# Kernel optimization log

Hardware: AMD Instinct MI355X
Metric: run time of the kernel (lower is better)

Reference implementation:

```python
import jax, jax.numpy as jnp
import numpy as np


def setup_inputs() -> dict:
    key = jax.random.key(0)
    k1, k2, k3 = jax.random.split(key, 3)
    d_in, d_sae, N = 2048, 16384, 8192
    x = jax.random.normal(k1, (N, d_in), dtype=jnp.float32)
    W_enc = jax.random.normal(k2, (d_in, d_sae), dtype=jnp.float32) * (1.0 / np.sqrt(d_in))
    W_dec = jax.random.normal(k3, (d_sae, d_in), dtype=jnp.float32)
    # normalize decoder rows (SAE convention; check_decoder_norms expects unit rows)
    W_dec = W_dec / jnp.linalg.norm(W_dec, axis=1, keepdims=True)
    b_enc = jnp.zeros((d_sae,), dtype=jnp.float32)
    b_dec = jnp.zeros((d_in,), dtype=jnp.float32)
    return {"x": x, "W_enc": W_enc, "W_dec": W_dec, "b_enc": b_enc, "b_dec": b_dec, "k": 64}


def reference(x, W_enc, W_dec, b_enc, b_dec, k):
    # encode: dense matmul then top-k masking with ReLU on kept activations
    pre_acts = x @ W_enc + b_enc                      # [N, d_sae]
    top_acts, top_idx = jax.lax.top_k(pre_acts, k)    # [N, k] each
    N = pre_acts.shape[0]
    rows = jnp.arange(N)[:, None]                     # [N, 1]
    acts = jnp.zeros_like(pre_acts).at[rows, top_idx].set(jax.nn.relu(top_acts))
    # decode
    recon = acts @ W_dec + b_dec                      # [N, d_in]
    return recon
```

## Files before the change

kernel.cpp:

```cpp
#include <hip/hip_runtime.h>

#define M_ROWS 8192
#define K_DIM  2048
#define N_SAE  16384
#define TOPK   64
#define WEPS   0.027f

typedef __attribute__((ext_vector_type(8))) short bf16x8;
typedef __attribute__((ext_vector_type(4))) float f32x4;

__device__ __forceinline__ unsigned short f2bf(float f) {
  unsigned u = __float_as_uint(f);
  u += 0x7FFFu + ((u >> 16) & 1u);
  return (unsigned short)(u >> 16);
}

__device__ __forceinline__ float key2float(unsigned k) {
  unsigned short bits = (k & 0x8000u) ? (unsigned short)(k ^ 0x8000u)
                                      : (unsigned short)(~k);
  _Float16 h;
  __builtin_memcpy(&h, &bits, 2);
  return (float)h;
}

__device__ __forceinline__ void gload16(const void* g, void* l) {
  __builtin_amdgcn_global_load_lds(
      (const __attribute__((address_space(1))) unsigned int*)g,
      (__attribute__((address_space(3))) unsigned int*)l, 16, 0, 0);
}

__global__ __launch_bounds__(256) void k_convx(const float* __restrict__ x,
                                               unsigned short* __restrict__ xb) {
  const long i = ((long)blockIdx.x * 256 + threadIdx.x) * 4;
  float4 v = *(const float4*)(x + i);
  ushort4 o;
  o.x = f2bf(v.x); o.y = f2bf(v.y); o.z = f2bf(v.z); o.w = f2bf(v.w);
  *(ushort4*)(xb + i) = o;
}

__global__ __launch_bounds__(256) void k_transpose(const float* __restrict__ W,
                                                   float* __restrict__ Wt,
                                                   unsigned short* __restrict__ Wtb) {
  __shared__ float tile[32][33];
  const int nb = blockIdx.x * 32;
  const int kb = blockIdx.y * 32;
  const int tx = threadIdx.x & 31;
  const int ty = threadIdx.x >> 5;
#pragma unroll
  for (int i = 0; i < 32; i += 8)
    tile[ty + i][tx] = W[(long)(kb + ty + i) * N_SAE + nb + tx];
  __syncthreads();
#pragma unroll
  for (int i = 0; i < 32; i += 8) {
    float v = tile[tx][ty + i];
    long o = (long)(nb + ty + i) * K_DIM + kb + tx;
    Wt[o] = v;
    Wtb[o] = f2bf(v);
  }
}

__global__ __launch_bounds__(256) void k_gemm(const unsigned short* __restrict__ A,
                                              const unsigned short* __restrict__ B,
                                              const float* __restrict__ b_enc,
                                              _Float16* __restrict__ C) {
  __shared__ unsigned short As[128 * 32];
  __shared__ unsigned short Bs[128 * 32];
  const int t = threadIdx.x;
  const int lane = t & 63;
  const int wave = t >> 6;
  const int wm = wave >> 1, wn = wave & 1;
  const int bm = blockIdx.y * 128, bn = blockIdx.x * 128;
  f32x4 acc[4][4] = {};

  const int c0 = t, c1 = t + 256;
  const unsigned short* a0 = A + (long)(bm + (c0 >> 2)) * K_DIM + (c0 & 3) * 8;
  const unsigned short* a1 = A + (long)(bm + (c1 >> 2)) * K_DIM + (c1 & 3) * 8;
  const unsigned short* b0 = B + (long)(bn + (c0 >> 2)) * K_DIM + (c0 & 3) * 8;
  const unsigned short* b1 = B + (long)(bn + (c1 >> 2)) * K_DIM + (c1 & 3) * 8;
  unsigned short* la0 = As + c0 * 8;
  unsigned short* la1 = As + c1 * 8;
  unsigned short* lb0 = Bs + c0 * 8;
  unsigned short* lb1 = Bs + c1 * 8;

  const int kh = lane >> 4;
  const int ml = lane & 15;

  for (int k0 = 0; k0 < K_DIM; k0 += 32) {
    __syncthreads();
    gload16(a0 + k0, la0);
    gload16(a1 + k0, la1);
    gload16(b0 + k0, lb0);
    gload16(b1 + k0, lb1);
    __syncthreads();
    bf16x8 af[4], bfr[4];
#pragma unroll
    for (int i = 0; i < 4; i++)
      af[i] = *(const bf16x8*)(As + (wm * 64 + i * 16 + ml) * 32 + kh * 8);
#pragma unroll
    for (int j = 0; j < 4; j++)
      bfr[j] = *(const bf16x8*)(Bs + (wn * 64 + j * 16 + ml) * 32 + kh * 8);
#pragma unroll
    for (int i = 0; i < 4; i++)
#pragma unroll
      for (int j = 0; j < 4; j++)
        acc[i][j] = __builtin_amdgcn_mfma_f32_16x16x32_bf16(af[i], bfr[j], acc[i][j], 0, 0, 0);
  }
#pragma unroll
  for (int j = 0; j < 4; j++) {
    const int gn = bn + wn * 64 + j * 16 + ml;
    const float bias = b_enc[gn];
#pragma unroll
    for (int i = 0; i < 4; i++) {
      const int gm0 = bm + wm * 64 + i * 16 + kh * 4;
#pragma unroll
      for (int r = 0; r < 4; r++)
        C[(long)(gm0 + r) * N_SAE + gn] = (_Float16)(acc[i][j][r] + bias);
    }
  }
}

__global__ __launch_bounds__(256) void k_select(const unsigned short* __restrict__ pre,
                                                int* __restrict__ def_idx,
                                                int* __restrict__ amb_idx,
                                                int* __restrict__ counts) {
  __shared__ unsigned short keys[16384];
  __shared__ unsigned int hist[256];
  __shared__ unsigned int scan[256];
  __shared__ unsigned int sc[8];
  const long row = blockIdx.x;
  const int t = threadIdx.x;
  const uint4* src = (const uint4*)(pre + row * N_SAE);
  uint4* kdst = (uint4*)keys;
#pragma unroll
  for (int i = 0; i < 8; i++) {
    uint4 v = src[i * 256 + t];
    uint4 o;
    unsigned s;
    s = v.x & 0x80008000u; o.x = v.x ^ (0x80008000u | ((s >> 15) * 0x7FFFu));
    s = v.y & 0x80008000u; o.y = v.y ^ (0x80008000u | ((s >> 15) * 0x7FFFu));
    s = v.z & 0x80008000u; o.z = v.z ^ (0x80008000u | ((s >> 15) * 0x7FFFu));
    s = v.w & 0x80008000u; o.w = v.w ^ (0x80008000u | ((s >> 15) * 0x7FFFu));
    kdst[i * 256 + t] = o;
  }
  hist[t] = 0;
  if (t < 8) sc[t] = 0;
  __syncthreads();
  for (int i = 0; i < 64; i++) {
    unsigned k = keys[i * 256 + t];
    atomicAdd(&hist[k >> 8], 1u);
  }
  __syncthreads();
  scan[t] = hist[t];
  __syncthreads();
  for (int off = 1; off < 256; off <<= 1) {
    unsigned v = (t + off < 256) ? scan[t + off] : 0u;
    __syncthreads();
    scan[t] += v;
    __syncthreads();
  }
  if (scan[t] >= TOPK && (t == 255 || scan[t + 1] < TOPK)) {
    sc[0] = (unsigned)t;
    sc[1] = (t == 255) ? 0u : scan[t + 1];
  }
  __syncthreads();
  const unsigned bstar = sc[0];
  const unsigned H = sc[1];
  hist[t] = 0;
  __syncthreads();
  for (int i = 0; i < 64; i++) {
    unsigned k = keys[i * 256 + t];
    if ((k >> 8) == bstar) atomicAdd(&hist[k & 255u], 1u);
  }
  __syncthreads();
  scan[t] = hist[t];
  __syncthreads();
  for (int off = 1; off < 256; off <<= 1) {
    unsigned v = (t + off < 256) ? scan[t + off] : 0u;
    __syncthreads();
    scan[t] += v;
    __syncthreads();
  }
  if (H + scan[t] >= TOPK && (t == 255 || H + scan[t + 1] < TOPK)) sc[2] = (unsigned)t;
  __syncthreads();
  const unsigned T = (bstar << 8) | sc[2];
  const float tf = key2float(T);
  const float lo = tf - WEPS;
  const float hi = tf + WEPS;
  for (int i = 0; i < 64; i++) {
    unsigned k = keys[i * 256 + t];
    float vf = key2float(k);
    if (vf > hi) {
      unsigned p = atomicAdd(&sc[3], 1u);
      def_idx[row * 64 + p] = i * 256 + t;
    } else if (vf >= lo) {
      unsigned p = atomicAdd(&sc[4], 1u);
      if (p < 64) amb_idx[row * 64 + p] = i * 256 + t;
    }
  }
  __syncthreads();
  if (t == 0) {
    counts[row * 2]     = (int)sc[3];
    counts[row * 2 + 1] = (int)(sc[4] < 64u ? sc[4] : 64u);
  }
}

__global__ __launch_bounds__(256) void k_exact2(const float* __restrict__ x,
                                                const float* __restrict__ Wt,
                                                const float* __restrict__ b_enc,
                                                const _Float16* __restrict__ pre,
                                                const int* __restrict__ def_idx,
                                                const int* __restrict__ amb_idx,
                                                const int* __restrict__ counts,
                                                int* __restrict__ tidx,
                                                float* __restrict__ tact) {
  __shared__ float xs[2048];
  __shared__ double vals[64];
  __shared__ int idxs[64];
  const int row = blockIdx.x;
  const int t = threadIdx.x;
  {
    const float4* src = (const float4*)(x + (long)row * K_DIM);
    ((float4*)xs)[t] = src[t];
    ((float4*)xs)[t + 256] = src[t + 256];
  }
  const int ndef = counts[row * 2];
  const int namb = counts[row * 2 + 1];
  if (t < 64) {
    idxs[t] = (t < namb) ? amb_idx[row * 64 + t] : -1;
    vals[t] = -1e300;
  }
  __syncthreads();
  const int wave = t >> 6, lane = t & 63;
  for (int c = wave; c < namb; c += 4) {
    const int f = idxs[c];
    const float4* w = (const float4*)(Wt + (long)f * K_DIM);
    const float4* xv4 = (const float4*)xs;
    double s = 0.0;
#pragma unroll
    for (int j = 0; j < 8; j++) {
      float4 wv = w[j * 64 + lane];
      float4 xv = xv4[j * 64 + lane];
      s += (double)wv.x * (double)xv.x;
      s += (double)wv.y * (double)xv.y;
      s += (double)wv.z * (double)xv.z;
      s += (double)wv.w * (double)xv.w;
    }
#pragma unroll
    for (int off = 32; off > 0; off >>= 1) s += __shfl_down(s, off);
    if (lane == 0) vals[c] = s + (double)b_enc[f];
  }
  __syncthreads();
  for (int kk = 2; kk <= 64; kk <<= 1) {
    for (int j = kk >> 1; j > 0; j >>= 1) {
      if (t < 64) {
        const int p = t ^ j;
        if (p > t) {
          const bool up = ((t & kk) == 0);
          double a = vals[t], b = vals[p];
          if (up ? (a < b) : (a > b)) {
            vals[t] = b; vals[p] = a;
            int tmp = idxs[t]; idxs[t] = idxs[p]; idxs[p] = tmp;
          }
        }
      }
      __syncthreads();
    }
  }
  if (t < ndef) {
    const int f = def_idx[row * 64 + t];
    const float v = (float)pre[(long)row * N_SAE + f];
    tidx[row * TOPK + t] = f;
    tact[row * TOPK + t] = v > 0.f ? v : 0.f;
  }
  const int need = TOPK - ndef;
  if (t < need) {
    int f = idxs[t];
    double v = vals[t];
    if (f < 0) { f = 0; v = 0.0; }
    tidx[row * TOPK + ndef + t] = f;
    tact[row * TOPK + ndef + t] = (float)(v > 0.0 ? v : 0.0);
  }
}

__global__ __launch_bounds__(256) void k_decode(const float* __restrict__ Wd,
                                                const float* __restrict__ b_dec,
                                                const int* __restrict__ tidx,
                                                const float* __restrict__ tact,
                                                float* __restrict__ out) {
  __shared__ int fid[TOPK];
  __shared__ float fac[TOPK];
  const int row = blockIdx.x, t = threadIdx.x;
  if (t < TOPK) {
    fid[t] = tidx[row * TOPK + t];
    fac[t] = tact[row * TOPK + t];
  }
  __syncthreads();
  float4 acc0 = ((const float4*)b_dec)[t * 2];
  float4 acc1 = ((const float4*)b_dec)[t * 2 + 1];
  for (int i = 0; i < TOPK; i++) {
    const float a = fac[i];
    const float4* w = (const float4*)(Wd + (long)fid[i] * K_DIM) + t * 2;
    float4 w0 = w[0], w1 = w[1];
    acc0.x += a * w0.x; acc0.y += a * w0.y; acc0.z += a * w0.z; acc0.w += a * w0.w;
    acc1.x += a * w1.x; acc1.y += a * w1.y; acc1.z += a * w1.z; acc1.w += a * w1.w;
  }
  float4* o = (float4*)(out + (long)row * K_DIM);
  o[t * 2] = acc0;
  o[t * 2 + 1] = acc1;
}

extern "C" void kernel_launch(void* const* d_in, const int* in_sizes, int n_in,
                              void* d_out, int out_size, void* d_ws, size_t ws_size,
                              hipStream_t stream) {
  const float* x     = (const float*)d_in[0];
  const float* W_enc = (const float*)d_in[1];
  const float* W_dec = (const float*)d_in[2];
  const float* b_enc = (const float*)d_in[3];
  const float* b_dec = (const float*)d_in[4];
  float* out = (float*)d_out;
  char* ws = (char*)d_ws;

  const size_t OFF_WT   = 0;
  const size_t OFF_XB   = 134217728;
  const size_t OFF_TIDX = 134217728;
  const size_t OFF_TACT = 136314880;
  const size_t OFF_WTB  = 167772160;
  const size_t OFF_PRE  = 234881024;
  const size_t OFF_DEF  = 503316480;
  const size_t OFF_AMB  = 505413632;
  const size_t OFF_CNT  = 507510784;

  float*          WencT = (float*)(ws + OFF_WT);
  unsigned short* xb    = (unsigned short*)(ws + OFF_XB);
  unsigned short* Wtb   = (unsigned short*)(ws + OFF_WTB);
  _Float16*       pre   = (_Float16*)(ws + OFF_PRE);
  int*            didx  = (int*)(ws + OFF_DEF);
  int*            aidx  = (int*)(ws + OFF_AMB);
  int*            cnt   = (int*)(ws + OFF_CNT);
  int*            tidx  = (int*)(ws + OFF_TIDX);
  float*          tact  = (float*)(ws + OFF_TACT);

  k_convx<<<M_ROWS * K_DIM / 1024, 256, 0, stream>>>(x, xb);
  k_transpose<<<dim3(N_SAE / 32, K_DIM / 32), 256, 0, stream>>>(W_enc, WencT, Wtb);
  k_gemm<<<dim3(N_SAE / 128, M_ROWS / 128), 256, 0, stream>>>(xb, Wtb, b_enc, pre);
  k_select<<<M_ROWS, 256, 0, stream>>>((const unsigned short*)pre, didx, aidx, cnt);
  k_exact2<<<M_ROWS, 256, 0, stream>>>(x, WencT, b_enc, pre, didx, aidx, cnt, tidx, tact);
  k_decode<<<M_ROWS, 256, 0, stream>>>(W_dec, b_dec, tidx, tact, out);
}
```

Baseline: 1.892 ms.

## Rewrite encoder GEMM with 256x256 tiles, 4-stage async LDS pipeline and swizzles

The bf16 encoder GEMM moves from 128x128 tiles with one LDS buffer and two barriers per k-step to 256x256 tiles with 512 threads. It uses a four-buffer LDS ring fed by direct global-to-LDS loads issued three stages ahead, and waits with explicit vmcnt counts so memory latency overlaps the MFMA work. It also adds an XOR swizzle on the LDS layout to avoid bank conflicts, a block-index swizzle for L2 locality, and raised wave priority around the MFMAs. The larger tile raises arithmetic intensity but uses 128 KB of LDS and many accumulator registers, which may limit occupancy.

```diff
diff --git a/kernel.cpp b/kernel.cpp
--- a/kernel.cpp
+++ b/kernel.cpp
@@ -59,62 +59,88 @@
   }
 }
 
-__global__ __launch_bounds__(256) void k_gemm(const unsigned short* __restrict__ A,
-                                              const unsigned short* __restrict__ B,
-                                              const float* __restrict__ b_enc,
-                                              _Float16* __restrict__ C) {
-  __shared__ unsigned short As[128 * 32];
-  __shared__ unsigned short Bs[128 * 32];
+__global__ __launch_bounds__(512, 2) void k_gemm(const unsigned short* __restrict__ A,
+                                                 const unsigned short* __restrict__ B,
+                                                 const float* __restrict__ b_enc,
+                                                 _Float16* __restrict__ C) {
+  __shared__ unsigned short lds[4 * 16384];
   const int t = threadIdx.x;
   const int lane = t & 63;
-  const int wave = t >> 6;
-  const int wm = wave >> 1, wn = wave & 1;
-  const int bm = blockIdx.y * 128, bn = blockIdx.x * 128;
-  f32x4 acc[4][4] = {};
-
-  const int c0 = t, c1 = t + 256;
-  const unsigned short* a0 = A + (long)(bm + (c0 >> 2)) * K_DIM + (c0 & 3) * 8;
-  const unsigned short* a1 = A + (long)(bm + (c1 >> 2)) * K_DIM + (c1 & 3) * 8;
-  const unsigned short* b0 = B + (long)(bn + (c0 >> 2)) * K_DIM + (c0 & 3) * 8;
-  const unsigned short* b1 = B + (long)(bn + (c1 >> 2)) * K_DIM + (c1 & 3) * 8;
-  unsigned short* la0 = As + c0 * 8;
-  unsigned short* la1 = As + c1 * 8;
-  unsigned short* lb0 = Bs + c0 * 8;
-  unsigned short* lb1 = Bs + c1 * 8;
-
-  const int kh = lane >> 4;
-  const int ml = lane & 15;
-
-  for (int k0 = 0; k0 < K_DIM; k0 += 32) {
-    __syncthreads();
-    gload16(a0 + k0, la0);
-    gload16(a1 + k0, la1);
-    gload16(b0 + k0, lb0);
-    gload16(b1 + k0, lb1);
-    __syncthreads();
-    bf16x8 af[4], bfr[4];
-#pragma unroll
-    for (int i = 0; i < 4; i++)
-      af[i] = *(const bf16x8*)(As + (wm * 64 + i * 16 + ml) * 32 + kh * 8);
-#pragma unroll
-    for (int j = 0; j < 4; j++)
-      bfr[j] = *(const bf16x8*)(Bs + (wn * 64 + j * 16 + ml) * 32 + kh * 8);
-#pragma unroll
-    for (int i = 0; i < 4; i++)
-#pragma unroll
-      for (int j = 0; j < 4; j++)
-        acc[i][j] = __builtin_amdgcn_mfma_f32_16x16x32_bf16(af[i], bfr[j], acc[i][j], 0, 0, 0);
-  }
-#pragma unroll
-  for (int j = 0; j < 4; j++) {
-    const int gn = bn + wn * 64 + j * 16 + ml;
+  const int w = t >> 6;
+  const int wm = w >> 2, wn = w & 3;
+  const int ml = lane & 15, kh = lane >> 4;
+
+  const int bid = blockIdx.x;
+  const int swz = (bid & 7) * 256 + (bid >> 3);
+  const int bn = (swz & 63) * 256;
+  const int bm = (swz >> 6) * 256;
+
+  const int r0 = t >> 2;
+  const int c0 = (t & 3) ^ (r0 & 3) ^ ((r0 >> 2) & 3);
+  const int r1 = r0 + 128;
+  const int c1 = (t & 3) ^ (r1 & 3) ^ ((r1 >> 2) & 3);
+  const unsigned short* gA0 = A + (long)(bm + r0) * K_DIM + c0 * 8;
+  const unsigned short* gA1 = A + (long)(bm + r1) * K_DIM + c1 * 8;
+  const unsigned short* gB0 = B + (long)(bn + r0) * K_DIM + c0 * 8;
+  const unsigned short* gB1 = B + (long)(bn + r1) * K_DIM + c1 * 8;
+  char* lb = (char*)lds;
+  const int dA0 = t * 16,          dA1 = 8192 + t * 16;
+  const int dB0 = 16384 + t * 16,  dB1 = 24576 + t * 16;
+
+  const int fx = (ml & 3) ^ ((ml >> 2) & 3);
+  const int offA0 = (wm * 128 + ml) * 64 + ((kh ^ fx) * 16);
+  const int offB0 = 16384 + (wn * 64 + ml) * 64 + ((kh ^ fx) * 16);
+
+  f32x4 acc[8][4] = {};
+
+#define STAGE(kt_) do {                         \
+    const int bb_ = ((kt_) & 3) * 32768;        \
+    const int ko_ = (kt_) * 32;                 \
+    gload16(gA0 + ko_, lb + bb_ + dA0);         \
+    gload16(gA1 + ko_, lb + bb_ + dA1);         \
+    gload16(gB0 + ko_, lb + bb_ + dB0);         \
+    gload16(gB1 + ko_, lb + bb_ + dB1);         \
+  } while (0)
+
+  STAGE(0);
+  asm volatile("" ::: "memory");
+  STAGE(1);
+  asm volatile("" ::: "memory");
+  STAGE(2);
+
+  for (int kt = 0; kt < 64; ++kt) {
+    if (kt < 62)       asm volatile("s_waitcnt vmcnt(8)" ::: "memory");
+    else if (kt == 62) asm volatile("s_waitcnt vmcnt(4)" ::: "memory");
+    else               asm volatile("s_waitcnt vmcnt(0)" ::: "memory");
+    __builtin_amdgcn_s_barrier();
+    asm volatile("" ::: "memory");
+    if (kt < 61) STAGE(kt + 3);
+    const char* bp = lb + (kt & 3) * 32768;
+    bf16x8 af[8], bv[4];
+#pragma unroll
+    for (int mi = 0; mi < 8; ++mi) af[mi] = *(const bf16x8*)(bp + offA0 + mi * 1024);
+#pragma unroll
+    for (int ni = 0; ni < 4; ++ni) bv[ni] = *(const bf16x8*)(bp + offB0 + ni * 1024);
+    __builtin_amdgcn_s_setprio(1);
+#pragma unroll
+    for (int mi = 0; mi < 8; ++mi)
+#pragma unroll
+      for (int ni = 0; ni < 4; ++ni)
+        acc[mi][ni] = __builtin_amdgcn_mfma_f32_16x16x32_bf16(af[mi], bv[ni], acc[mi][ni], 0, 0, 0);
+    __builtin_amdgcn_s_setprio(0);
+  }
+#undef STAGE
+
+#pragma unroll
+  for (int ni = 0; ni < 4; ++ni) {
+    const int gn = bn + wn * 64 + ni * 16 + ml;
     const float bias = b_enc[gn];
 #pragma unroll
-    for (int i = 0; i < 4; i++) {
-      const int gm0 = bm + wm * 64 + i * 16 + kh * 4;
-#pragma unroll
-      for (int r = 0; r < 4; r++)
-        C[(long)(gm0 + r) * N_SAE + gn] = (_Float16)(acc[i][j][r] + bias);
+    for (int mi = 0; mi < 8; ++mi) {
+      const int gm0 = bm + wm * 128 + mi * 16 + kh * 4;
+#pragma unroll
+      for (int rr = 0; rr < 4; ++rr)
+        C[(long)(gm0 + rr) * N_SAE + gn] = (_Float16)(acc[mi][ni][rr] + bias);
     }
   }
 }
@@ -342,7 +368,7 @@
 
   k_convx<<<M_ROWS * K_DIM / 1024, 256, 0, stream>>>(x, xb);
   k_transpose<<<dim3(N_SAE / 32, K_DIM / 32), 256, 0, stream>>>(W_enc, WencT, Wtb);
-  k_gemm<<<dim3(N_SAE / 128, M_ROWS / 128), 256, 0, stream>>>(xb, Wtb, b_enc, pre);
+  k_gemm<<<2048, 512, 0, stream>>>(xb, Wtb, b_enc, pre);
   k_select<<<M_ROWS, 256, 0, stream>>>((const unsigned short*)pre, didx, aidx, cnt);
   k_exact2<<<M_ROWS, 256, 0, stream>>>(x, WencT, b_enc, pre, didx, aidx, cnt, tidx, tact);
   k_decode<<<M_ROWS, 256, 0, stream>>>(W_dec, b_dec, tidx, tact, out);
```

New measurement: 1.841 ms. 2.7% less time.
